# Optimization experiments

Measured on AMD Instinct MI355X. Metric: run time of the kernel, lower is better.

The kernel has to match this reference:

```python
import jax, jax.numpy as jnp
import numpy as np

NUM_LEVELS = 3
K = 512
COMMIT = (0.25, 0.5, 1.0)
DECAY = 0.99
EPS = 1e-05


def setup_inputs() -> dict:
    key = jax.random.key(0)
    k1, k2, k3 = jax.random.split(key, 3)
    z_e = jax.random.normal(k1, (16, 4096, 1024), dtype=jnp.float32)
    codebooks = jax.random.normal(k2, (NUM_LEVELS, K, 1024), dtype=jnp.float32)
    ema_cluster = jnp.ones((NUM_LEVELS, K), dtype=jnp.float32)
    ema_w = jax.random.normal(k3, (NUM_LEVELS, K, 1024), dtype=jnp.float32)
    return {"z_e": z_e, "codebooks": codebooks, "ema_cluster": ema_cluster, "ema_w": ema_w}


def reference(z_e, codebooks, ema_cluster, ema_w):
    """Hierarchical residual VQ: 3 levels of cdist+argmin+gather, residual subtract,
    commitment loss, and EMA codebook update stats via scatter-add (segment_sum)."""
    B, T, D = z_e.shape
    flat = z_e.reshape(-1, D)  # [N, D]
    residual = flat
    z_q = jnp.zeros_like(flat)
    loss = jnp.zeros((), dtype=flat.dtype)
    idx_list = []
    new_codebooks = []

    for l in range(NUM_LEVELS):
        C = codebooks[l]  # [K, D]
        # squared euclidean distances [N, K] (expanded form, no NxKxD intermediate)
        d = (jnp.sum(residual * residual, axis=-1, keepdims=True)
             - 2.0 * residual @ C.T
             + jnp.sum(C * C, axis=-1))
        idx = jnp.argmin(d, axis=-1)  # [N] nearest code
        q = C[idx]  # gather [N, D]

        # commitment loss (EMA-style VQ: no gradient codebook loss)
        loss = loss + COMMIT[l] * jnp.mean((residual - jax.lax.stop_gradient(q)) ** 2)

        # EMA codebook update statistics (scatter-add, no grad)
        r_sg = jax.lax.stop_gradient(residual)
        counts = jax.ops.segment_sum(jnp.ones((r_sg.shape[0],), dtype=flat.dtype), idx, num_segments=K)
        sums = jax.ops.segment_sum(r_sg, idx, num_segments=K)  # [K, D]
        cs = DECAY * ema_cluster[l] + (1.0 - DECAY) * counts
        w = DECAY * ema_w[l] + (1.0 - DECAY) * sums
        n = jnp.sum(cs)
        cs_norm = (cs + EPS) / (n + K * EPS) * n  # laplace smoothing
        new_codebooks.append(w / cs_norm[:, None])

        residual = residual - q
        z_q = z_q + q
        idx_list.append(idx)

    # straight-through estimator
    z_q_st = flat + jax.lax.stop_gradient(z_q - flat)
    indices = jnp.stack(idx_list).reshape(NUM_LEVELS, B, T)
    return z_q_st.reshape(B, T, D), loss, indices, jnp.stack(new_codebooks)
```

## Files before the change

kernel.cpp:

```cpp
#include <hip/hip_runtime.h>

#define NPTS   65536
#define DIM    1024
#define NCODE  512
#define NLVL   3

#define ZQ_OFF   0
#define LOSS_OFF 67108864
#define IDX_OFF  67108865
#define CB_OFF   67305473

#define PB    128
#define CBCH  256
#define KS    32
#define NTHR2 512

typedef unsigned short u16;
typedef unsigned int   u32;
typedef __attribute__((ext_vector_type(8))) short short8;
typedef __attribute__((ext_vector_type(4))) float f32x4;

__device__ inline void merge_top2(float& v1, int& i1, float& v2, int& i2,
                                  float w1, int j1, float w2, int j2) {
    bool aFirst = (v1 < w1) || (v1 == w1 && i1 < j1);
    float t1v = aFirst ? v1 : w1; int t1i = aFirst ? i1 : j1;
    float c1v = aFirst ? v2 : w2; int c1i = aFirst ? i2 : j2;
    float c2v = aFirst ? w1 : v1; int c2i = aFirst ? j1 : i1;
    bool cFirst = (c1v < c2v) || (c1v == c2v && c1i < c2i);
    v1 = t1v; i1 = t1i;
    v2 = cFirst ? c1v : c2v;
    i2 = cFirst ? c1i : c2i;
}

__device__ inline u16 bf16_rne(float x) {
    u32 u = __float_as_uint(x);
    u32 r = u + 0x7fffu + ((u >> 16) & 1u);
    return (u16)(r >> 16);
}
__device__ inline float bf16_f(u16 h) { return __uint_as_float(((u32)h) << 16); }

__device__ inline void gload_lds16(const void* g, void* l) {
    __builtin_amdgcn_global_load_lds((const __attribute__((address_space(1))) void*)g,
                                     (__attribute__((address_space(3))) void*)l, 16, 0, 0);
}

__global__ __launch_bounds__(256) void cnorm_kernel(const float* __restrict__ cb,
                                                    float* __restrict__ cnorm) {
    __shared__ float sd[256];
    const int b = blockIdx.x;
    const int tid = threadIdx.x;
    const float4 v = *(const float4*)&cb[(size_t)b * DIM + tid * 4];
    sd[tid] = v.x*v.x + v.y*v.y + v.z*v.z + v.w*v.w;
    __syncthreads();
    for (int o = 128; o > 0; o >>= 1) { if (tid < o) sd[tid] += sd[tid+o]; __syncthreads(); }
    if (tid == 0) cnorm[b] = sd[0];
}

__global__ __launch_bounds__(256) void cvtcb_kernel(const float* __restrict__ cbs,
                                                    char* __restrict__ planes) {
    const int b = blockIdx.x;
    const int tid = threadIdx.x;
    const int l = b >> 9, k = b & 511;
    u16* ph = (u16*)(planes + (size_t)l * 2097152);
    u16* pl = ph + NCODE * DIM;
    const float4 v = *(const float4*)&cbs[(size_t)b * DIM + tid * 4];
    float xs[4] = {v.x, v.y, v.z, v.w};
    u16 hh[4], ll[4];
    #pragma unroll
    for (int e = 0; e < 4; ++e) {
        hh[e] = bf16_rne(xs[e]);
        ll[e] = bf16_rne(xs[e] - bf16_f(hh[e]));
    }
    *(ushort4*)&ph[(size_t)k * DIM + tid * 4] = make_ushort4(hh[0], hh[1], hh[2], hh[3]);
    *(ushort4*)&pl[(size_t)k * DIM + tid * 4] = make_ushort4(ll[0], ll[1], ll[2], ll[3]);
}

__global__ __launch_bounds__(512, 4) void level_kernel(
        const float* __restrict__ r_in,
        float* __restrict__ r_out,
        const float* __restrict__ cbf,
        const u16* __restrict__ cb_h,
        const u16* __restrict__ cb_l,
        const float* __restrict__ cnorm_l,
        float* __restrict__ out_idx_f,
        int*   __restrict__ ws_idx,
        float* __restrict__ loss_partial)
{
    __shared__ union {
        struct {
            u16 A[2][CBCH][KS];
            u16 B[2][PB][KS];
        } st;
        struct {
            float4 top[4][PB];
            double ref[PB][2][2];
            int    i1[PB], i2[PB], w[PB];
            float  red[NTHR2];
        } tl;
    } sm;
    __shared__ float s_cn[NCODE];

    const int tid  = threadIdx.x;
    const int lane = tid & 63;
    const int wid  = tid >> 6;
    const int wm   = wid >> 1;
    const int wn   = wid & 1;
    const int g    = lane >> 4;
    const int l15  = lane & 15;
    const int fr   = (l15 >> 1) & 3;
    const int pbase = blockIdx.x * PB;

    u16* sAf = &sm.st.A[0][0][0];
    u16* sBf = &sm.st.B[0][0][0];

    s_cn[tid] = cnorm_l[tid];

    float bv1[4], bv2[4]; int bi1[4], bi2[4];
    #pragma unroll
    for (int i = 0; i < 4; ++i) { bv1[i] = 1e30f; bv2[i] = 1e30f; bi1[i] = 0; bi2[i] = 1; }

    const u16* srcp = (wid < 4) ? cb_h : cb_l;

    for (int ch = 0; ch < 2; ++ch) {
        const int cbase = ch * CBCH;
        f32x4 acc[4][4] = {};

        for (int ks0 = 0; ks0 < DIM; ks0 += KS) {
            __syncthreads();

            #pragma unroll
            for (int j = 0; j < 4; ++j) {
                const int c   = wid * 256 + j * 64 + lane;
                const int cc  = c & 1023;
                const int row = cc >> 2, slot = cc & 3;
                const u16* gp = srcp + (size_t)(cbase + row) * DIM + ks0
                                + ((slot ^ ((row >> 1) & 3)) << 3);
                gload_lds16(gp, sAf + (size_t)c * 8);
            }

            {
                const int row = tid >> 2, slot = tid & 3;
                const float* gp = r_in + (size_t)(pbase + row) * DIM + ks0 + slot * 8;
                const float4 a0 = *(const float4*)gp;
                const float4 a1 = *(const float4*)(gp + 4);
                float xs[8] = {a0.x, a0.y, a0.z, a0.w, a1.x, a1.y, a1.z, a1.w};
                short8 h8, l8;
                #pragma unroll
                for (int e = 0; e < 8; ++e) {
                    const u16 hb = bf16_rne(xs[e]);
                    const u16 lb = bf16_rne(xs[e] - bf16_f(hb));
                    h8[e] = (short)hb; l8[e] = (short)lb;
                }
                const int woff = row * KS + ((slot ^ ((row >> 1) & 3)) << 3);
                *(short8*)(sBf + woff) = h8;
                *(short8*)(sBf + 4096 + woff) = l8;
            }
            asm volatile("s_waitcnt vmcnt(0)" ::: "memory");
            __syncthreads();

            {
                const int ksl = (g ^ fr) << 3;
                short8 bh[4], bl[4];
                #pragma unroll
                for (int nf = 0; nf < 4; ++nf) {
                    const int row = wn * 64 + nf * 16 + l15;
                    bh[nf] = *(const short8*)(sBf + row * KS + ksl);
                    bl[nf] = *(const short8*)(sBf + 4096 + row * KS + ksl);
                }
                #pragma unroll
                for (int mf = 0; mf < 4; ++mf) {
                    const int row = wm * 64 + mf * 16 + l15;
                    const short8 ah = *(const short8*)(sAf + row * KS + ksl);
                    const short8 al = *(const short8*)(sAf + 8192 + row * KS + ksl);
                    #pragma unroll
                    for (int nf = 0; nf < 4; ++nf) {
                        acc[mf][nf] = __builtin_amdgcn_mfma_f32_16x16x32_bf16(ah, bh[nf], acc[mf][nf], 0, 0, 0);
                        acc[mf][nf] = __builtin_amdgcn_mfma_f32_16x16x32_bf16(ah, bl[nf], acc[mf][nf], 0, 0, 0);
                        acc[mf][nf] = __builtin_amdgcn_mfma_f32_16x16x32_bf16(al, bh[nf], acc[mf][nf], 0, 0, 0);
                    }
                }
            }
        }

        #pragma unroll
        for (int nf = 0; nf < 4; ++nf)
            #pragma unroll
            for (int mf = 0; mf < 4; ++mf)
                #pragma unroll
                for (int r = 0; r < 4; ++r) {
                    const int code = cbase + wm * 64 + mf * 16 + g * 4 + r;
                    const float sv = s_cn[code] - 2.0f * acc[mf][nf][r];
                    if (sv < bv1[nf])      { bv2[nf] = bv1[nf]; bi2[nf] = bi1[nf]; bv1[nf] = sv; bi1[nf] = code; }
                    else if (sv < bv2[nf]) { bv2[nf] = sv; bi2[nf] = code; }
                }
    }

    __syncthreads();

    #pragma unroll
    for (int nf = 0; nf < 4; ++nf) {
        float v1 = bv1[nf], v2 = bv2[nf]; int i1 = bi1[nf], i2 = bi2[nf];
        #pragma unroll
        for (int m = 16; m < 64; m <<= 1) {
            const float w1 = __shfl_xor(v1, m); const int j1 = __shfl_xor(i1, m);
            const float w2 = __shfl_xor(v2, m); const int j2 = __shfl_xor(i2, m);
            merge_top2(v1, i1, v2, i2, w1, j1, w2, j2);
        }
        if (g == 0)
            sm.tl.top[wm][wn * 64 + nf * 16 + l15] =
                make_float4(v1, __int_as_float(i1), v2, __int_as_float(i2));
    }
    __syncthreads();

    if (tid < PB) {
        float4 t = sm.tl.top[0][tid];
        float v1 = t.x; int i1 = __float_as_int(t.y);
        float v2 = t.z; int i2 = __float_as_int(t.w);
        #pragma unroll
        for (int wmm = 1; wmm < 4; ++wmm) {
            const float4 u = sm.tl.top[wmm][tid];
            merge_top2(v1, i1, v2, i2, u.x, __float_as_int(u.y), u.z, __float_as_int(u.w));
        }
        sm.tl.i1[tid] = i1; sm.tl.i2[tid] = i2;
    }
    __syncthreads();

    {
        const int p = tid >> 2, cand = (tid >> 1) & 1, half = tid & 1;
        const int k = cand ? sm.tl.i2[p] : sm.tl.i1[p];
        const float4* rr = (const float4*)(r_in + (size_t)(pbase + p) * DIM + half * 512);
        const float4* cr = (const float4*)(cbf + (size_t)k * DIM + half * 512);
        double s0 = 0.0, s1 = 0.0, s2 = 0.0, s3 = 0.0;
        for (int d = 0; d < 128; ++d) {
            const float4 c4 = cr[d];
            const float4 r4 = rr[d];
            s0 += (double)c4.x * ((double)c4.x - 2.0 * (double)r4.x);
            s1 += (double)c4.y * ((double)c4.y - 2.0 * (double)r4.y);
            s2 += (double)c4.z * ((double)c4.z - 2.0 * (double)r4.z);
            s3 += (double)c4.w * ((double)c4.w - 2.0 * (double)r4.w);
        }
        sm.tl.ref[p][cand][half] = (s0 + s1) + (s2 + s3);
    }
    __syncthreads();
    if (tid < PB) {
        const double sA_ = sm.tl.ref[tid][0][0] + sm.tl.ref[tid][0][1];
        const double sB_ = sm.tl.ref[tid][1][0] + sm.tl.ref[tid][1][1];
        const int iA = sm.tl.i1[tid], iB = sm.tl.i2[tid];
        const int w = (sB_ < sA_ || (sB_ == sA_ && iB < iA)) ? iB : iA;
        sm.tl.w[tid] = w;
        out_idx_f[pbase + tid] = (float)w;
        ws_idx[pbase + tid] = w;
    }
    __syncthreads();

    float lsum = 0.f;
    const int colb = (tid & 255) * 4;
    const int phh  = tid >> 8;
    for (int pp = 0; pp < PB; pp += 2) {
        const int p = pp + phh;
        const int w = sm.tl.w[p];
        const size_t off = (size_t)(pbase + p) * DIM + colb;
        const float4 rv = *(const float4*)&r_in[off];
        const float4 cv = *(const float4*)&cbf[(size_t)w * DIM + colb];
        float4 rn;
        rn.x = rv.x - cv.x; rn.y = rv.y - cv.y; rn.z = rv.z - cv.z; rn.w = rv.w - cv.w;
        if (r_out) *(float4*)&r_out[off] = rn;
        lsum += rn.x*rn.x + rn.y*rn.y + rn.z*rn.z + rn.w*rn.w;
    }
    sm.tl.red[tid] = lsum;
    __syncthreads();
    for (int o = 256; o > 0; o >>= 1) { if (tid < o) sm.tl.red[tid] += sm.tl.red[tid + o]; __syncthreads(); }
    if (tid == 0) loss_partial[blockIdx.x] = sm.tl.red[0];
}

#define SCHUNK 4096
__global__ __launch_bounds__(256) void sums_kernel(
        const int* __restrict__ idx, const float* __restrict__ src,
        const float* __restrict__ cb, int addC,
        float* __restrict__ sums_out, int* __restrict__ counts_out)
{
    __shared__ int s_idx[SCHUNK];
    __shared__ int s_list[SCHUNK];
    __shared__ int s_scan[256];
    const int k = blockIdx.x, tid = threadIdx.x;
    float4 acc = make_float4(0.f, 0.f, 0.f, 0.f);
    int nk = 0;
    for (int base = 0; base < NPTS; base += SCHUNK) {
        __syncthreads();
        for (int j = tid; j < SCHUNK; j += 256) s_idx[j] = idx[base + j];
        __syncthreads();
        int cnt = 0;
        const int S = SCHUNK / 256;
        #pragma unroll
        for (int j = 0; j < S; ++j) cnt += (s_idx[tid * S + j] == k);
        s_scan[tid] = cnt;
        __syncthreads();
        for (int off = 1; off < 256; off <<= 1) {
            int v = (tid >= off) ? s_scan[tid - off] : 0;
            __syncthreads();
            s_scan[tid] += v;
            __syncthreads();
        }
        const int total = s_scan[255];
        int pos = s_scan[tid] - cnt;
        for (int j = 0; j < S; ++j)
            if (s_idx[tid * S + j] == k) s_list[pos++] = base + tid * S + j;
        __syncthreads();
        for (int j = 0; j < total; ++j) {
            const int pid = s_list[j];
            float4 v = *(const float4*)&src[(size_t)pid * DIM + tid * 4];
            acc.x += v.x; acc.y += v.y; acc.z += v.z; acc.w += v.w;
        }
        nk += total;
    }
    if (addC) {
        float4 c = *(const float4*)&cb[(size_t)k * DIM + tid * 4];
        float fn = (float)nk;
        acc.x += fn * c.x; acc.y += fn * c.y; acc.z += fn * c.z; acc.w += fn * c.w;
    }
    *(float4*)&sums_out[(size_t)k * DIM + tid * 4] = acc;
    if (tid == 0) counts_out[k] = nk;
}

__global__ __launch_bounds__(256) void zq_kernel(const float* __restrict__ z_e,
                                                 const float* __restrict__ cb2,
                                                 const int* __restrict__ idx2,
                                                 float* __restrict__ zq) {
    const int total = NPTS * (DIM / 4);
    for (int i = blockIdx.x * 256 + threadIdx.x; i < total; i += gridDim.x * 256) {
        const size_t e = (size_t)i * 4;
        const int p = (int)(e >> 10);
        const int d = (int)(e & 1023);
        const int w = idx2[p];
        float4 z = *(const float4*)&z_e[e];
        float4 r = *(const float4*)&zq[e];
        float4 c = *(const float4*)&cb2[(size_t)w * DIM + d];
        float4 o;
        o.x = z.x - r.x + c.x; o.y = z.y - r.y + c.y;
        o.z = z.z - r.z + c.z; o.w = z.w - r.w + c.w;
        *(float4*)&zq[e] = o;
    }
}

__global__ __launch_bounds__(512) void nsum_kernel(const float* __restrict__ ec,
                                                   const int* __restrict__ counts,
                                                   float* __restrict__ n_ws) {
    __shared__ float sd[512];
    const int l = blockIdx.x, tid = threadIdx.x;
    sd[tid] = 0.99f * ec[l * NCODE + tid] + 0.01f * (float)counts[l * NCODE + tid];
    __syncthreads();
    for (int o = 256; o > 0; o >>= 1) { if (tid < o) sd[tid] += sd[tid+o]; __syncthreads(); }
    if (tid == 0) n_ws[l] = sd[0];
}

__global__ __launch_bounds__(256) void newcb_kernel(const float* __restrict__ ema_w,
                                                    const float* __restrict__ sums,
                                                    const float* __restrict__ ec,
                                                    const int* __restrict__ counts,
                                                    const float* __restrict__ n_ws,
                                                    float* __restrict__ out_cb) {
    const int b = blockIdx.x;
    const int tid = threadIdx.x;
    const int l = b >> 9;
    const float cs = 0.99f * ec[b] + 0.01f * (float)counts[b];
    const float n = n_ws[l];
    const float csn = (cs + 1e-5f) / (n + 512.0f * 1e-5f) * n;
    const size_t off = (size_t)b * DIM + tid * 4;
    float4 w = *(const float4*)&ema_w[off];
    float4 s4 = *(const float4*)&sums[off];
    float4 o;
    o.x = (0.99f * w.x + 0.01f * s4.x) / csn;
    o.y = (0.99f * w.y + 0.01f * s4.y) / csn;
    o.z = (0.99f * w.z + 0.01f * s4.z) / csn;
    o.w = (0.99f * w.w + 0.01f * s4.w) / csn;
    *(float4*)&out_cb[off] = o;
}

__global__ __launch_bounds__(256) void loss_kernel(const float* __restrict__ lp,
                                                   float* __restrict__ out_loss) {
    __shared__ double sd[256];
    const int tid = threadIdx.x;
    const double commit[3] = {0.25, 0.5, 1.0};
    double acc = 0.0;
    for (int l = 0; l < NLVL; ++l) {
        double s = 0.0;
        for (int j = tid; j < 512; j += 256) s += (double)lp[l * 512 + j];
        sd[tid] = s;
        __syncthreads();
        for (int o = 128; o > 0; o >>= 1) { if (tid < o) sd[tid] += sd[tid+o]; __syncthreads(); }
        if (tid == 0) acc += commit[l] * sd[0] / 67108864.0;
        __syncthreads();
    }
    if (tid == 0) *out_loss = (float)acc;
}

extern "C" void kernel_launch(void* const* d_in, const int* in_sizes, int n_in,
                              void* d_out, int out_size, void* d_ws, size_t ws_size,
                              hipStream_t stream) {
    const float* z_e   = (const float*)d_in[0];
    const float* cbs   = (const float*)d_in[1];
    const float* ema_c = (const float*)d_in[2];
    const float* ema_w = (const float*)d_in[3];
    float* out = (float*)d_out;

    char* ws = (char*)d_ws;
    int*   ws_idx = (int*)ws;
    float* cnorm  = (float*)(ws + 786432);
    int*   counts = (int*)(ws + 792576);
    float* lossp  = (float*)(ws + 798720);
    float* n_ws   = (float*)(ws + 811008);
    float* sums   = (float*)(ws + 811024);
    char*  planes = (char*)(ws + 811024);

    float* zq       = out + ZQ_OFF;
    float* out_loss = out + LOSS_OFF;
    float* out_idx  = out + IDX_OFF;
    float* out_cb   = out + CB_OFF;

    const float* cb0 = cbs;
    const float* cb1 = cbs + (size_t)1 * NCODE * DIM;
    const float* cb2 = cbs + (size_t)2 * NCODE * DIM;

    u16* ph0 = (u16*)(planes);                     u16* pl0 = ph0 + NCODE * DIM;
    u16* ph1 = (u16*)(planes + 2097152);           u16* pl1 = ph1 + NCODE * DIM;
    u16* ph2 = (u16*)(planes + 2 * 2097152);       u16* pl2 = ph2 + NCODE * DIM;

    cvtcb_kernel<<<NLVL * NCODE, 256, 0, stream>>>(cbs, planes);
    cnorm_kernel<<<NLVL * NCODE, 256, 0, stream>>>(cbs, cnorm);

    level_kernel<<<NPTS / PB, NTHR2, 0, stream>>>(z_e, zq, cb0, ph0, pl0, cnorm,
                                                  out_idx, ws_idx, lossp);
    sums_kernel<<<NCODE, 256, 0, stream>>>(ws_idx, z_e, nullptr, 0,
                                           sums, counts);
    level_kernel<<<NPTS / PB, NTHR2, 0, stream>>>(zq, zq, cb1, ph1, pl1, cnorm + NCODE,
                                                  out_idx + NPTS, ws_idx + NPTS, lossp + 512);
    sums_kernel<<<NCODE, 256, 0, stream>>>(ws_idx + NPTS, zq, cb1, 1,
                                           sums + (size_t)NCODE * DIM, counts + NCODE);
    level_kernel<<<NPTS / PB, NTHR2, 0, stream>>>(zq, nullptr, cb2, ph2, pl2, cnorm + 2 * NCODE,
                                                  out_idx + 2 * NPTS, ws_idx + 2 * NPTS, lossp + 1024);
    sums_kernel<<<NCODE, 256, 0, stream>>>(ws_idx + 2 * NPTS, zq, nullptr, 0,
                                           sums + (size_t)2 * NCODE * DIM, counts + 2 * NCODE);
    zq_kernel<<<4096, 256, 0, stream>>>(z_e, cb2, ws_idx + 2 * NPTS, zq);

    nsum_kernel<<<NLVL, 512, 0, stream>>>(ema_c, counts, n_ws);
    newcb_kernel<<<NLVL * NCODE, 256, 0, stream>>>(ema_w, sums, ema_c, counts, n_ws, out_cb);
    loss_kernel<<<1, 256, 0, stream>>>(lossp, out_loss);
}
```

Baseline: 2.648 ms.

## Split sums gather across wavefronts with 8-row batched loads and LDS reduction

The per-code sums kernel now gives each wavefront its own subset of assigned points, and each lane covers four column slices of a row. Every wavefront issues eight rows' worth of float4 loads at once before accumulating, which raises memory-level parallelism over the old one-row-at-a-time dependent loop. Partial sums from the four wavefronts are combined through LDS at the end, and launch bounds now request two blocks per CU. This costs more registers and extra shared memory, and changes the floating-point summation order.

```diff
diff --git a/kernel.cpp b/kernel.cpp
--- a/kernel.cpp
+++ b/kernel.cpp
@@ -274,7 +274,7 @@
 }
 
 #define SCHUNK 4096
-__global__ __launch_bounds__(256) void sums_kernel(
+__global__ __launch_bounds__(256, 2) void sums_kernel(
         const int* __restrict__ idx, const float* __restrict__ src,
         const float* __restrict__ cb, int addC,
         float* __restrict__ sums_out, int* __restrict__ counts_out)
@@ -282,8 +282,14 @@
     __shared__ int s_idx[SCHUNK];
     __shared__ int s_list[SCHUNK];
     __shared__ int s_scan[256];
+    __shared__ float s_acc[3][DIM];
     const int k = blockIdx.x, tid = threadIdx.x;
-    float4 acc = make_float4(0.f, 0.f, 0.f, 0.f);
+    const int lane = tid & 63, w = tid >> 6;
+
+    float4 acc[4];
+    #pragma unroll
+    for (int q = 0; q < 4; ++q) acc[q] = make_float4(0.f, 0.f, 0.f, 0.f);
+
     int nk = 0;
     for (int base = 0; base < NPTS; base += SCHUNK) {
         __syncthreads();
@@ -306,20 +312,81 @@
         for (int j = 0; j < S; ++j)
             if (s_idx[tid * S + j] == k) s_list[pos++] = base + tid * S + j;
         __syncthreads();
-        for (int j = 0; j < total; ++j) {
-            const int pid = s_list[j];
-            float4 v = *(const float4*)&src[(size_t)pid * DIM + tid * 4];
-            acc.x += v.x; acc.y += v.y; acc.z += v.z; acc.w += v.w;
+
+        for (int jb = w * 8; jb < total; jb += 32) {
+            if (jb + 8 <= total) {
+                const float* p0 = src + (size_t)s_list[jb + 0] * DIM + lane * 4;
+                const float* p1 = src + (size_t)s_list[jb + 1] * DIM + lane * 4;
+                const float* p2 = src + (size_t)s_list[jb + 2] * DIM + lane * 4;
+                const float* p3 = src + (size_t)s_list[jb + 3] * DIM + lane * 4;
+                const float* p4 = src + (size_t)s_list[jb + 4] * DIM + lane * 4;
+                const float* p5 = src + (size_t)s_list[jb + 5] * DIM + lane * 4;
+                const float* p6 = src + (size_t)s_list[jb + 6] * DIM + lane * 4;
+                const float* p7 = src + (size_t)s_list[jb + 7] * DIM + lane * 4;
+                float4 ld0[4], ld1[4], ld2[4], ld3[4], ld4[4], ld5[4], ld6[4], ld7[4];
+                #pragma unroll
+                for (int q = 0; q < 4; ++q) {
+                    ld0[q] = *(const float4*)(p0 + q * 256);
+                    ld1[q] = *(const float4*)(p1 + q * 256);
+                    ld2[q] = *(const float4*)(p2 + q * 256);
+                    ld3[q] = *(const float4*)(p3 + q * 256);
+                    ld4[q] = *(const float4*)(p4 + q * 256);
+                    ld5[q] = *(const float4*)(p5 + q * 256);
+                    ld6[q] = *(const float4*)(p6 + q * 256);
+                    ld7[q] = *(const float4*)(p7 + q * 256);
+                }
+                #pragma unroll
+                for (int q = 0; q < 4; ++q) {
+                    acc[q].x += ld0[q].x; acc[q].y += ld0[q].y; acc[q].z += ld0[q].z; acc[q].w += ld0[q].w;
+                    acc[q].x += ld1[q].x; acc[q].y += ld1[q].y; acc[q].z += ld1[q].z; acc[q].w += ld1[q].w;
+                    acc[q].x += ld2[q].x; acc[q].y += ld2[q].y; acc[q].z += ld2[q].z; acc[q].w += ld2[q].w;
+                    acc[q].x += ld3[q].x; acc[q].y += ld3[q].y; acc[q].z += ld3[q].z; acc[q].w += ld3[q].w;
+                    acc[q].x += ld4[q].x; acc[q].y += ld4[q].y; acc[q].z += ld4[q].z; acc[q].w += ld4[q].w;
+                    acc[q].x += ld5[q].x; acc[q].y += ld5[q].y; acc[q].z += ld5[q].z; acc[q].w += ld5[q].w;
+                    acc[q].x += ld6[q].x; acc[q].y += ld6[q].y; acc[q].z += ld6[q].z; acc[q].w += ld6[q].w;
+                    acc[q].x += ld7[q].x; acc[q].y += ld7[q].y; acc[q].z += ld7[q].z; acc[q].w += ld7[q].w;
+                }
+            } else {
+                for (int jr = jb; jr < total; ++jr) {
+                    const float* p = src + (size_t)s_list[jr] * DIM + lane * 4;
+                    #pragma unroll
+                    for (int q = 0; q < 4; ++q) {
+                        const float4 v = *(const float4*)(p + q * 256);
+                        acc[q].x += v.x; acc[q].y += v.y; acc[q].z += v.z; acc[q].w += v.w;
+                    }
+                }
+            }
         }
         nk += total;
     }
-    if (addC) {
-        float4 c = *(const float4*)&cb[(size_t)k * DIM + tid * 4];
-        float fn = (float)nk;
-        acc.x += fn * c.x; acc.y += fn * c.y; acc.z += fn * c.z; acc.w += fn * c.w;
-    }
-    *(float4*)&sums_out[(size_t)k * DIM + tid * 4] = acc;
-    if (tid == 0) counts_out[k] = nk;
+
+    if (w > 0) {
+        #pragma unroll
+        for (int q = 0; q < 4; ++q)
+            *(float4*)&s_acc[w - 1][q * 256 + lane * 4] = acc[q];
+    }
+    __syncthreads();
+    if (w == 0) {
+        #pragma unroll
+        for (int q = 0; q < 4; ++q) {
+            const int col = q * 256 + lane * 4;
+            float4 a = acc[q];
+            const float4 b1 = *(const float4*)&s_acc[0][col];
+            const float4 b2 = *(const float4*)&s_acc[1][col];
+            const float4 b3 = *(const float4*)&s_acc[2][col];
+            a.x = ((a.x + b1.x) + b2.x) + b3.x;
+            a.y = ((a.y + b1.y) + b2.y) + b3.y;
+            a.z = ((a.z + b1.z) + b2.z) + b3.z;
+            a.w = ((a.w + b1.w) + b2.w) + b3.w;
+            if (addC) {
+                const float4 c4 = *(const float4*)&cb[(size_t)k * DIM + col];
+                const float fn = (float)nk;
+                a.x += fn * c4.x; a.y += fn * c4.y; a.z += fn * c4.z; a.w += fn * c4.w;
+            }
+            *(float4*)&sums_out[(size_t)k * DIM + col] = a;
+        }
+        if (tid == 0) counts_out[k] = nk;
+    }
 }
 
 __global__ __launch_bounds__(256) void zq_kernel(const float* __restrict__ z_e,
```

Result: slower. 3.010 ms (+13.6%).
